# Kernel optimization log

Hardware: AMD Instinct MI355X
Metric: run time of the kernel (lower is better)

The kernel has to match this reference:

```python
import jax, jax.numpy as jnp
import numpy as np

NUM_HEADS = 16


def setup_inputs() -> dict:
    key = jax.random.key(0)
    ks = jax.random.split(key, 4)
    B, N, C = 4, 1024, 1024
    H, D = NUM_HEADS, C // NUM_HEADS
    L_cache = 4096
    x = jax.random.normal(ks[0], (B, N, C), dtype=jnp.float32)
    kv_cache = jax.random.normal(ks[1], (2, B, H, L_cache, D), dtype=jnp.float32)
    w_qkv = jax.random.normal(ks[2], (C, 3 * C), dtype=jnp.float32) * (C ** -0.5)
    w_proj = jax.random.normal(ks[3], (C, C), dtype=jnp.float32) * (C ** -0.5)
    b_proj = jnp.zeros((C,), dtype=jnp.float32)
    return {"x": x, "kv_cache": kv_cache, "w_qkv": w_qkv, "w_proj": w_proj, "b_proj": b_proj}


def reference(x, kv_cache, w_qkv, w_proj, b_proj):
    B, N, C = x.shape
    H = NUM_HEADS
    D = C // H
    scale = D ** -0.5
    # QKV projection (no bias), split into q,k,v with shape [B,H,N,D]
    qkv = (x @ w_qkv).reshape(B, N, 3, H, D).transpose(2, 0, 3, 1, 4)
    q, k, v = qkv[0], qkv[1], qkv[2]
    # concat KV cache along sequence axis -> [B,H,L_cache+N,D]
    k = jnp.concatenate([kv_cache[0], k], axis=2)
    v = jnp.concatenate([kv_cache[1], v], axis=2)
    # scaled dot-product attention (no causal mask, eval mode: no dropout)
    attn = jax.nn.softmax(jnp.einsum('bhnd,bhld->bhnl', q * scale, k), axis=-1)
    out = jnp.einsum('bhnl,bhld->bhnd', attn, v)  # [B,H,N,D]
    out = out.transpose(0, 2, 1, 3).reshape(B, N, C)
    return out @ w_proj + b_proj
```

## Files before the change

### kernel.cpp

```cpp
#include <hip/hip_runtime.h>

typedef short  s16x8 __attribute__((ext_vector_type(8)));
typedef float  f32x4 __attribute__((ext_vector_type(4)));

#define B_   4
#define N_   1024
#define C_   1024
#define H_   16
#define D_   64
#define LC_  4096
#define LT_  5120
#define KVHALF_ 16777216

#define SM_C1 0.18033688011f
#define SM_C2 20.1977305724f

static __device__ __forceinline__ unsigned short f2bf(float x) {
    union { float f; unsigned int u; } c; c.f = x;
    unsigned int r = (c.u + 0x7FFFu + ((c.u >> 16) & 1u)) >> 16;
    return (unsigned short)r;
}
static __device__ __forceinline__ unsigned int pk2(float lo, float hi) {
    union { float f; unsigned int u; } cl, ch;
    cl.f = lo; ch.f = hi;
    return __builtin_amdgcn_perm(ch.u + 0x8000u, cl.u + 0x8000u, 0x07060302u);
}
static __device__ __forceinline__ s16x8 cvt8f(const float* p) {
    f32x4 a = *(const f32x4*)p;
    f32x4 b = *(const f32x4*)(p + 4);
    s16x8 r;
#pragma unroll
    for (int j = 0; j < 4; ++j) {
        r[j]     = (short)f2bf(a[j]);
        r[j + 4] = (short)f2bf(b[j]);
    }
    return r;
}
static __device__ __forceinline__ f32x4 mfma16(s16x8 a, s16x8 b, f32x4 c) {
    return __builtin_amdgcn_mfma_f32_16x16x32_bf16(a, b, c, 0, 0, 0);
}

static __device__ __forceinline__ int vt_addr(int d, int k) {
    return d * 72 + ((((k >> 3) ^ ((d >> 3) & 7)) & 7) << 3) + (k & 7);
}
static __device__ __forceinline__ int bt_addr(int n, int k) {
    return n * 40 + ((((k >> 3) ^ (n >> 3)) & 3) << 3) + (k & 7);
}

__global__ __launch_bounds__(256) void convert_bf(const float* __restrict__ src,
                                                  unsigned short* __restrict__ dst,
                                                  int total8)
{
    size_t stride = (size_t)gridDim.x * blockDim.x;
    for (size_t i = blockIdx.x * blockDim.x + threadIdx.x; i < (size_t)total8; i += stride)
        *(s16x8*)(dst + i * 8) = cvt8f(src + i * 8);
}

__global__ __launch_bounds__(256) void transpose_v(const float* __restrict__ vsrc,
                                                   unsigned short* __restrict__ vdst)
{
    __shared__ __attribute__((aligned(16))) unsigned short tlds[64 * 72];
    const int tid = threadIdx.x;
    const int bh = blockIdx.x >> 6;
    const int l0 = (blockIdx.x & 63) * 64;
    {
        const int lrow = tid >> 2, d0 = (tid & 3) * 16;
        const float* p = vsrc + ((size_t)bh * LC_ + l0 + lrow) * D_ + d0;
        s16x8 a = cvt8f(p), b = cvt8f(p + 8);
#pragma unroll
        for (int j = 0; j < 8; ++j) {
            tlds[vt_addr(d0 + j, lrow)]     = (unsigned short)a[j];
            tlds[vt_addr(d0 + 8 + j, lrow)] = (unsigned short)b[j];
        }
    }
    __syncthreads();
    {
        const int d = tid >> 2, lo = (tid & 3) * 16;
        const int kb = lo >> 3, sd = (d >> 3) & 7;
        s16x8 v0 = *(const s16x8*)&tlds[d * 72 + ((kb ^ sd) << 3)];
        s16x8 v1 = *(const s16x8*)&tlds[d * 72 + (((kb + 1) ^ sd) << 3)];
        unsigned short* q = vdst + ((size_t)bh * D_ + d) * LC_ + l0 + lo;
        *(s16x8*)q = v0;
        *(s16x8*)(q + 8) = v1;
    }
}

template <int NN, int KK>
__global__ __launch_bounds__(256) void transpose_w(const float* __restrict__ src,
                                                   unsigned short* __restrict__ dst)
{
    __shared__ __attribute__((aligned(16))) unsigned short tlds[64 * 72];
    const int tid = threadIdx.x;
    const int n0 = blockIdx.x * 64;
    const int k0 = blockIdx.y * 64;
    {
        const int kl = tid >> 2, c0 = (tid & 3) * 16;
        const float* p = src + (size_t)(k0 + kl) * NN + n0 + c0;
        s16x8 a = cvt8f(p), b = cvt8f(p + 8);
#pragma unroll
        for (int j = 0; j < 8; ++j) {
            tlds[vt_addr(c0 + j, kl)]     = (unsigned short)a[j];
            tlds[vt_addr(c0 + 8 + j, kl)] = (unsigned short)b[j];
        }
    }
    __syncthreads();
    {
        const int nl = tid >> 2, ko = (tid & 3) * 16;
        const int kb = ko >> 3, sd = (nl >> 3) & 7;
        s16x8 v0 = *(const s16x8*)&tlds[nl * 72 + ((kb ^ sd) << 3)];
        s16x8 v1 = *(const s16x8*)&tlds[nl * 72 + (((kb + 1) ^ sd) << 3)];
        unsigned short* q = dst + (size_t)(n0 + nl) * KK + k0 + ko;
        *(s16x8*)q = v0;
        *(s16x8*)(q + 8) = v1;
    }
}

template <int NW, int MODE>
__global__ __launch_bounds__(256) void gemm_bt(
    const unsigned short* __restrict__ A,
    const unsigned short* __restrict__ BwT,
    const float* __restrict__ bias,
    unsigned short* __restrict__ out0,
    unsigned short* __restrict__ out1,
    unsigned short* __restrict__ out2,
    float* __restrict__ outf,
    int K)
{
    __shared__ __attribute__((aligned(16))) unsigned short Alds[64 * 40];
    __shared__ __attribute__((aligned(16))) unsigned short BT[64 * 40];

    const int tid = threadIdx.x;
    const int w  = tid >> 6;
    const int l  = tid & 63;
    const int g  = l >> 4;
    const int li = l & 15;
    const int bm = blockIdx.y * 64;
    const int bn = blockIdx.x * 64;

    f32x4 acc[4] = {};

    for (int k0 = 0; k0 < K; k0 += 32) {
        {
            int row = tid >> 2, ko = (tid & 3) * 8;
            *(s16x8*)&Alds[row * 40 + ko] =
                *(const s16x8*)(A + (size_t)(bm + row) * K + k0 + ko);
        }
        {
            int n = tid >> 2, kh = (tid & 3) * 8;
            *(s16x8*)&BT[bt_addr(n, kh)] =
                *(const s16x8*)(BwT + (size_t)(bn + n) * K + k0 + kh);
        }
        __syncthreads();

        s16x8 a = *(const s16x8*)&Alds[(w * 16 + li) * 40 + g * 8];
#pragma unroll
        for (int ct = 0; ct < 4; ++ct) {
            s16x8 b = *(const s16x8*)&BT[bt_addr(ct * 16 + li, g * 8)];
            acc[ct] = mfma16(a, b, acc[ct]);
        }
        __syncthreads();
    }

    if (MODE == 0) {
        const int which = bn >> 10;
        const int h     = (bn & 1023) >> 6;
        const int b     = bm >> 10;
#pragma unroll
        for (int ct = 0; ct < 4; ++ct) {
            const int d = ct * 16 + li;
#pragma unroll
            for (int r = 0; r < 4; ++r) {
                int m = bm + w * 16 + g * 4 + r;
                int n = m & 1023;
                unsigned short val = f2bf(acc[ct][r]);
                if (which == 0)
                    out0[((size_t)((b * H_ + h) * N_ + n)) * D_ + d] = val;
                else if (which == 1)
                    out1[((size_t)((b * H_ + h) * N_ + n)) * D_ + d] = val;
                else
                    out2[((size_t)((b * H_ + h) * D_ + d)) * N_ + n] = val;
            }
        }
    } else {
#pragma unroll
        for (int ct = 0; ct < 4; ++ct) {
            const int c = bn + ct * 16 + li;
            const float bv = bias[c];
#pragma unroll
            for (int r = 0; r < 4; ++r) {
                int m = bm + w * 16 + g * 4 + r;
                outf[(size_t)m * NW + c] = acc[ct][r] + bv;
            }
        }
    }
}

__global__ __launch_bounds__(256) void attn_single(
    const unsigned short* __restrict__ qbuf,
    const unsigned short* __restrict__ knew,
    const unsigned short* __restrict__ vnewT,
    const unsigned short* __restrict__ kcbf,
    const unsigned short* __restrict__ vtcbf,
    unsigned short* __restrict__ x2)
{
    __shared__ __attribute__((aligned(16))) unsigned short Klds[64 * 72];
    __shared__ __attribute__((aligned(16))) unsigned short VT[64 * 72];

    const int tid  = threadIdx.x;
    const int w    = tid >> 6;
    const int l    = tid & 63;
    const int g    = l >> 4;
    const int li   = l & 15;

    const int i0   = blockIdx.x;
    const int xcd  = i0 & 7;
    const int j0   = i0 >> 3;
    const int bh   = xcd * 8 + (j0 >> 4);
    const int qblk = j0 & 15;

    s16x8 ones;
    {
        const short ov = (li == 0) ? (short)0x3F80 : (short)0;
#pragma unroll
        for (int j = 0; j < 8; ++j) ones[j] = ov;
    }

    const unsigned short* qrowp =
        qbuf + ((size_t)bh * N_ + qblk * 64 + w * 16 + li) * D_;
    const s16x8 qf0 = *(const s16x8*)(qrowp + g * 8);
    const s16x8 qf1 = *(const s16x8*)(qrowp + 32 + g * 8);

    f32x4 acc[5] = {};

    const int kr = tid >> 2;
    const int ko = (tid & 3) * 16;
    s16x8 kreg0, kreg1, vreg0, vreg1;

    auto LOAD = [&](int t) {
        const int key0 = t * 64;
        if (t < LC_ / 64) {
            const unsigned short* ks = kcbf + ((size_t)bh * LC_ + key0 + kr) * D_ + ko;
            kreg0 = *(const s16x8*)ks; kreg1 = *(const s16x8*)(ks + 8);
            const unsigned short* vs = vtcbf + ((size_t)bh * D_ + kr) * LC_ + key0 + ko;
            vreg0 = *(const s16x8*)vs; vreg1 = *(const s16x8*)(vs + 8);
        } else {
            const unsigned short* ks = knew + ((size_t)bh * N_ + (key0 - LC_) + kr) * D_ + ko;
            kreg0 = *(const s16x8*)ks; kreg1 = *(const s16x8*)(ks + 8);
            const unsigned short* vs = vnewT + ((size_t)bh * D_ + kr) * N_ + (key0 - LC_) + ko;
            vreg0 = *(const s16x8*)vs; vreg1 = *(const s16x8*)(vs + 8);
        }
    };
    LOAD(0);

    const int kb  = ko >> 3;
    const int sdw = (kr >> 3) & 7;

    for (int t = 0; t < LT_ / 64; ++t) {
        __syncthreads();
        *(s16x8*)&Klds[kr * 72 + ko]     = kreg0;
        *(s16x8*)&Klds[kr * 72 + ko + 8] = kreg1;
        *(s16x8*)&VT[kr * 72 + ((kb ^ sdw) << 3)]       = vreg0;
        *(s16x8*)&VT[kr * 72 + (((kb + 1) ^ sdw) << 3)] = vreg1;
        if (t + 1 < LT_ / 64) LOAD(t + 1);
        __syncthreads();

        f32x4 sc[4];
#pragma unroll
        for (int ct = 0; ct < 4; ++ct) {
            f32x4 s = {};
            s16x8 ka0 = *(const s16x8*)&Klds[(ct * 16 + li) * 72 + g * 8];
            s16x8 ka1 = *(const s16x8*)&Klds[(ct * 16 + li) * 72 + 32 + g * 8];
            s = mfma16(ka0, qf0, s);
            sc[ct] = mfma16(ka1, qf1, s);
        }

        unsigned int pk[4][2];
#pragma unroll
        for (int ct = 0; ct < 4; ++ct) {
            float p0 = exp2f(fmaf(sc[ct][0], SM_C1, -SM_C2));
            float p1 = exp2f(fmaf(sc[ct][1], SM_C1, -SM_C2));
            float p2 = exp2f(fmaf(sc[ct][2], SM_C1, -SM_C2));
            float p3 = exp2f(fmaf(sc[ct][3], SM_C1, -SM_C2));
            pk[ct][0] = pk2(p0, p1);
            pk[ct][1] = pk2(p2, p3);
        }

        unsigned int a0 = pk[0][0], b0 = pk[1][0];
        asm("v_permlane32_swap_b32 %0, %1" : "+v"(a0), "+v"(b0));
        asm("v_permlane16_swap_b32 %0, %1" : "+v"(a0), "+v"(b0));
        unsigned int a1 = pk[0][1], b1 = pk[1][1];
        asm("v_permlane32_swap_b32 %0, %1" : "+v"(a1), "+v"(b1));
        asm("v_permlane16_swap_b32 %0, %1" : "+v"(a1), "+v"(b1));
        unsigned int c0 = pk[2][0], e0 = pk[3][0];
        asm("v_permlane32_swap_b32 %0, %1" : "+v"(c0), "+v"(e0));
        asm("v_permlane16_swap_b32 %0, %1" : "+v"(c0), "+v"(e0));
        unsigned int c1 = pk[2][1], e1 = pk[3][1];
        asm("v_permlane32_swap_b32 %0, %1" : "+v"(c1), "+v"(e1));
        asm("v_permlane16_swap_b32 %0, %1" : "+v"(c1), "+v"(e1));

        union { unsigned int u[4]; s16x8 v; } P0, P1;
        P0.u[0] = a0; P0.u[1] = a1; P0.u[2] = b0; P0.u[3] = b1;
        P1.u[0] = c0; P1.u[1] = c1; P1.u[2] = e0; P1.u[3] = e1;
        const s16x8 pf0 = P0.v, pf1 = P1.v;

#pragma unroll
        for (int dt = 0; dt < 4; ++dt) {
            const int vrow = dt * 16 + li;
            const int sd = (vrow >> 3) & 7;
            s16x8 vb0 = *(const s16x8*)&VT[vrow * 72 + ((g ^ sd) << 3)];
            s16x8 vb1 = *(const s16x8*)&VT[vrow * 72 + (((4 + g) ^ sd) << 3)];
            acc[dt] = mfma16(pf0, vb0, acc[dt]);
            acc[dt] = mfma16(pf1, vb1, acc[dt]);
        }
        acc[4] = mfma16(pf0, ones, acc[4]);
        acc[4] = mfma16(pf1, ones, acc[4]);
    }

    float linv[4];
#pragma unroll
    for (int r = 0; r < 4; ++r)
        linv[r] = 1.0f / __shfl(acc[4][r], l & 48);
    const int b = bh >> 4, h = bh & 15;
#pragma unroll
    for (int dt = 0; dt < 4; ++dt) {
#pragma unroll
        for (int r = 0; r < 4; ++r) {
            int qrow = qblk * 64 + w * 16 + g * 4 + r;
            x2[((size_t)(b * N_ + qrow)) * C_ + h * D_ + dt * 16 + li] =
                f2bf(acc[dt][r] * linv[r]);
        }
    }
}

extern "C" void kernel_launch(void* const* d_in, const int* in_sizes, int n_in,
                              void* d_out, int out_size, void* d_ws, size_t ws_size,
                              hipStream_t stream)
{
    const float* x      = (const float*)d_in[0];
    const float* kv     = (const float*)d_in[1];
    const float* w_qkv  = (const float*)d_in[2];
    const float* w_proj = (const float*)d_in[3];
    const float* b_proj = (const float*)d_in[4];
    float* out = (float*)d_out;

    unsigned short* kcbf  = (unsigned short*)d_ws;
    unsigned short* vtcbf = kcbf + KVHALF_;
    unsigned short* q     = vtcbf + KVHALF_;
    unsigned short* knew  = q + 4194304;
    unsigned short* vnewT = knew + 4194304;
    unsigned short* tail  = vnewT + 4194304;

    unsigned short* xbf = tail;
    unsigned short* x2  = tail;
    unsigned short* wqT = tail + 4194304;
    unsigned short* wpT = tail + 4194304;

    convert_bf<<<dim3(2048), 256, 0, stream>>>(x, xbf, 524288);
    transpose_w<3072, 1024><<<dim3(48, 16), 256, 0, stream>>>(w_qkv, wqT);
    convert_bf<<<dim3(2048), 256, 0, stream>>>(kv, kcbf, KVHALF_ / 8);
    transpose_v<<<dim3(64 * 64), 256, 0, stream>>>(kv + KVHALF_, vtcbf);

    gemm_bt<3072, 0><<<dim3(48, 64), 256, 0, stream>>>(
        xbf, wqT, nullptr, q, knew, vnewT, nullptr, C_);

    attn_single<<<dim3(B_ * H_ * (N_ / 64)), 256, 0, stream>>>(
        q, knew, vnewT, kcbf, vtcbf, x2);

    transpose_w<1024, 1024><<<dim3(16, 16), 256, 0, stream>>>(w_proj, wpT);
    gemm_bt<1024, 1><<<dim3(16, 64), 256, 0, stream>>>(
        x2, wpT, b_proj, nullptr, nullptr, nullptr, out, C_);
}
```

Before: 304.9 us.

## Enlarge GEMM block tile to 128x128 with 2x2 warp grid and 4x4 MFMA per wave

The bf16 GEMM kernel used for both the QKV and output projections now computes a 128x128 output tile per block instead of 64x64. Each wave owns a 64x64 sub-tile and issues a 4x4 grid of MFMAs per K step, reusing A and B fragments from registers. This raises arithmetic intensity and cuts global and LDS traffic per flop. In exchange it uses more accumulator registers and LDS and launches fewer blocks: 768 for QKV and 256 for the output projection, which may underfill the GPU.

```diff
diff --git a/kernel.cpp b/kernel.cpp
--- a/kernel.cpp
+++ b/kernel.cpp
@@ -116,7 +116,7 @@
 }
 
 template <int NW, int MODE>
-__global__ __launch_bounds__(256) void gemm_bt(
+__global__ __launch_bounds__(256) void gemm128(
     const unsigned short* __restrict__ A,
     const unsigned short* __restrict__ BwT,
     const float* __restrict__ bias,
@@ -126,70 +126,88 @@
     float* __restrict__ outf,
     int K)
 {
-    __shared__ __attribute__((aligned(16))) unsigned short Alds[64 * 40];
-    __shared__ __attribute__((aligned(16))) unsigned short BT[64 * 40];
+    __shared__ __attribute__((aligned(16))) unsigned short Alds[128 * 40];
+    __shared__ __attribute__((aligned(16))) unsigned short BT[128 * 40];
 
     const int tid = threadIdx.x;
     const int w  = tid >> 6;
     const int l  = tid & 63;
     const int g  = l >> 4;
     const int li = l & 15;
-    const int bm = blockIdx.y * 64;
-    const int bn = blockIdx.x * 64;
-
-    f32x4 acc[4] = {};
+    const int wr = w >> 1;
+    const int wc = w & 1;
+    const int bm = blockIdx.y * 128;
+    const int bn = blockIdx.x * 128;
+
+    f32x4 acc[4][4] = {};
+
+    const int srow = tid >> 1;
+    const int sko  = (tid & 1) * 16;
 
     for (int k0 = 0; k0 < K; k0 += 32) {
         {
-            int row = tid >> 2, ko = (tid & 3) * 8;
-            *(s16x8*)&Alds[row * 40 + ko] =
-                *(const s16x8*)(A + (size_t)(bm + row) * K + k0 + ko);
+            const unsigned short* p = A + (size_t)(bm + srow) * K + k0 + sko;
+            *(s16x8*)&Alds[srow * 40 + sko]     = *(const s16x8*)p;
+            *(s16x8*)&Alds[srow * 40 + sko + 8] = *(const s16x8*)(p + 8);
         }
         {
-            int n = tid >> 2, kh = (tid & 3) * 8;
-            *(s16x8*)&BT[bt_addr(n, kh)] =
-                *(const s16x8*)(BwT + (size_t)(bn + n) * K + k0 + kh);
+            const unsigned short* p = BwT + (size_t)(bn + srow) * K + k0 + sko;
+            *(s16x8*)&BT[bt_addr(srow, sko)]     = *(const s16x8*)p;
+            *(s16x8*)&BT[bt_addr(srow, sko + 8)] = *(const s16x8*)(p + 8);
         }
         __syncthreads();
 
-        s16x8 a = *(const s16x8*)&Alds[(w * 16 + li) * 40 + g * 8];
-#pragma unroll
-        for (int ct = 0; ct < 4; ++ct) {
-            s16x8 b = *(const s16x8*)&BT[bt_addr(ct * 16 + li, g * 8)];
-            acc[ct] = mfma16(a, b, acc[ct]);
-        }
+        s16x8 ar[4], br[4];
+#pragma unroll
+        for (int i = 0; i < 4; ++i)
+            ar[i] = *(const s16x8*)&Alds[(wr * 64 + i * 16 + li) * 40 + g * 8];
+#pragma unroll
+        for (int j = 0; j < 4; ++j)
+            br[j] = *(const s16x8*)&BT[bt_addr(wc * 64 + j * 16 + li, g * 8)];
+#pragma unroll
+        for (int i = 0; i < 4; ++i)
+#pragma unroll
+            for (int j = 0; j < 4; ++j)
+                acc[i][j] = mfma16(ar[i], br[j], acc[i][j]);
         __syncthreads();
     }
 
     if (MODE == 0) {
         const int which = bn >> 10;
-        const int h     = (bn & 1023) >> 6;
         const int b     = bm >> 10;
 #pragma unroll
-        for (int ct = 0; ct < 4; ++ct) {
-            const int d = ct * 16 + li;
-#pragma unroll
-            for (int r = 0; r < 4; ++r) {
-                int m = bm + w * 16 + g * 4 + r;
-                int n = m & 1023;
-                unsigned short val = f2bf(acc[ct][r]);
-                if (which == 0)
-                    out0[((size_t)((b * H_ + h) * N_ + n)) * D_ + d] = val;
-                else if (which == 1)
-                    out1[((size_t)((b * H_ + h) * N_ + n)) * D_ + d] = val;
-                else
-                    out2[((size_t)((b * H_ + h) * D_ + d)) * N_ + n] = val;
+        for (int j = 0; j < 4; ++j) {
+            const int c = (bn & 1023) + wc * 64 + j * 16 + li;
+            const int h = c >> 6;
+            const int d = c & 63;
+#pragma unroll
+            for (int i = 0; i < 4; ++i) {
+#pragma unroll
+                for (int r = 0; r < 4; ++r) {
+                    const int m = bm + wr * 64 + i * 16 + g * 4 + r;
+                    const int n = m & 1023;
+                    unsigned short val = f2bf(acc[i][j][r]);
+                    if (which == 0)
+                        out0[((size_t)((b * H_ + h) * N_ + n)) * D_ + d] = val;
+                    else if (which == 1)
+                        out1[((size_t)((b * H_ + h) * N_ + n)) * D_ + d] = val;
+                    else
+                        out2[((size_t)((b * H_ + h) * D_ + d)) * N_ + n] = val;
+                }
             }
         }
     } else {
 #pragma unroll
-        for (int ct = 0; ct < 4; ++ct) {
-            const int c = bn + ct * 16 + li;
+        for (int j = 0; j < 4; ++j) {
+            const int c = bn + wc * 64 + j * 16 + li;
             const float bv = bias[c];
 #pragma unroll
-            for (int r = 0; r < 4; ++r) {
-                int m = bm + w * 16 + g * 4 + r;
-                outf[(size_t)m * NW + c] = acc[ct][r] + bv;
+            for (int i = 0; i < 4; ++i) {
+#pragma unroll
+                for (int r = 0; r < 4; ++r) {
+                    const int m = bm + wr * 64 + i * 16 + g * 4 + r;
+                    outf[(size_t)m * NW + c] = acc[i][j][r] + bv;
+                }
             }
         }
     }
@@ -360,13 +378,13 @@
     convert_bf<<<dim3(2048), 256, 0, stream>>>(kv, kcbf, KVHALF_ / 8);
     transpose_v<<<dim3(64 * 64), 256, 0, stream>>>(kv + KVHALF_, vtcbf);
 
-    gemm_bt<3072, 0><<<dim3(48, 64), 256, 0, stream>>>(
+    gemm128<3072, 0><<<dim3(24, 32), 256, 0, stream>>>(
         xbf, wqT, nullptr, q, knew, vnewT, nullptr, C_);
 
     attn_single<<<dim3(B_ * H_ * (N_ / 64)), 256, 0, stream>>>(
         q, knew, vnewT, kcbf, vtcbf, x2);
 
     transpose_w<1024, 1024><<<dim3(16, 16), 256, 0, stream>>>(w_proj, wpT);
-    gemm_bt<1024, 1><<<dim3(16, 64), 256, 0, stream>>>(
+    gemm128<1024, 1><<<dim3(8, 32), 256, 0, stream>>>(
         x2, wpT, b_proj, nullptr, nullptr, nullptr, out, C_);
 }
```

Result: faster. 292.2 us (-4.2%).
